# Kernel optimization log

Measured on AMD Instinct MI355X. Metric: run time of the kernel, lower is better.

The kernel has to match this reference:

```python
import jax, jax.numpy as jnp
import numpy as np

EPS = 1e-5

def conv1x1(x, w):
    # x: [B,C,H,W], w: [O,C] -> [B,O,H,W]
    return jnp.einsum('oc,bchw->bohw', w, x)

def bn(x, g, b, m, v):
    # inference batchnorm over channel dim 1
    scale = g / jnp.sqrt(v + EPS)
    return x * scale[None, :, None, None] + (b - m * scale)[None, :, None, None]

def setup_inputs() -> dict:
    key = jax.random.key(0)
    ks = jax.random.split(key, 20)
    B, Cin, S = 32, 256, 32
    C = Cin // 2
    rn = lambda k, sh: jax.random.normal(k, sh, dtype=jnp.float32)
    ru = lambda k, sh: jax.random.uniform(k, sh, dtype=jnp.float32)
    return {
        'x': rn(ks[0], (B, Cin, S, S)),
        'w1': rn(ks[1], (C, Cin)) * 0.05,
        'bn1_g': ru(ks[2], (C,)) + 0.5,
        'bn1_b': rn(ks[3], (C,)) * 0.1,
        'bn1_m': rn(ks[4], (C,)) * 0.1,
        'bn1_v': ru(ks[5], (C,)) + 0.5,
        'wq': rn(ks[6], (C, C)) * 0.05,
        'bq': rn(ks[7], (C,)) * 0.05,
        'wk': rn(ks[8], (C, C)) * 0.05,
        'bk': rn(ks[9], (C,)) * 0.05,
        'wv': rn(ks[10], (C, C)) * 0.05,
        'bv': rn(ks[11], (C,)) * 0.05,
        'rel_h': rn(ks[12], (1, C, S, 1)),
        'rel_w': rn(ks[13], (1, C, 1, S)),
        'w2': rn(ks[14], (Cin, C)) * 0.05,
        'bn2_g': ru(ks[15], (Cin,)) + 0.5,
        'bn2_b': rn(ks[16], (Cin,)) * 0.1,
        'bn2_m': rn(ks[17], (Cin,)) * 0.1,
        'bn2_v': ru(ks[18], (Cin,)) + 0.5,
    }

def reference(x, w1, bn1_g, bn1_b, bn1_m, bn1_v, wq, bq, wk, bk, wv, bv,
              rel_h, rel_w, w2, bn2_g, bn2_b, bn2_m, bn2_v):
    # cv1: 1x1 conv -> BN -> SiLU
    x1 = jax.nn.silu(bn(conv1x1(x, w1), bn1_g, bn1_b, bn1_m, bn1_v))
    B, C, H, W = x1.shape
    N = H * W
    # q/k/v: 1x1 conv with bias, flattened to [B,C,N]
    q = (conv1x1(x1, wq) + bq[None, :, None, None]).reshape(B, C, N)
    k = (conv1x1(x1, wk) + bk[None, :, None, None]).reshape(B, C, N)
    v = (conv1x1(x1, wv) + bv[None, :, None, None]).reshape(B, C, N)
    # content-content: q^T k -> [B,N,N]
    content_content = jnp.einsum('bci,bcj->bij', q, k)
    # content-position: pos^T q -> [B,N,N]
    pos = (rel_h + rel_w).reshape(C, N)  # [C,N]
    content_position = jnp.einsum('ci,bcj->bij', pos, q)
    attention = jax.nn.softmax(content_content + content_position, axis=-1)
    # out[b,c,i] = sum_j v[b,c,j] * attention[b,i,j]
    out = jnp.einsum('bcj,bij->bci', v, attention).reshape(B, C, H, W)
    # cv2: 1x1 conv -> BN -> SiLU, plus residual shortcut
    y = jax.nn.silu(bn(conv1x1(out, w2), bn2_g, bn2_b, bn2_m, bn2_v))
    return x + y
```

## Files before the change

kernel.cpp:

```cpp
#include <hip/hip_runtime.h>
#include <stdint.h>

typedef __bf16 bf16x8 __attribute__((ext_vector_type(8)));
typedef float  f32x4  __attribute__((ext_vector_type(4)));
typedef float  f32x16 __attribute__((ext_vector_type(16)));

#define MFMA(a,b,c)   __builtin_amdgcn_mfma_f32_16x16x32_bf16((a),(b),(c),0,0,0)
#define MFMA32(a,b,c) __builtin_amdgcn_mfma_f32_32x32x16_bf16((a),(b),(c),0,0,0)

__device__ __forceinline__ short f2b(float x) {
  uint32_t u = __float_as_uint(x);
  uint32_t r = (u + 0x7fffu + ((u >> 16) & 1u)) >> 16;
  return (short)r;
}

__device__ __forceinline__ uint32_t cvtpk(float lo, float hi) {
  uint32_t w;
  asm("v_cvt_pk_bf16_f32 %0, %1, %2" : "=v"(w) : "v"(lo), "v"(hi));
  return w;
}

__device__ __forceinline__ void glds16(const void* g, void* l) {
  __builtin_amdgcn_global_load_lds(
      (const __attribute__((address_space(1))) void*)(uintptr_t)g,
      (__attribute__((address_space(3))) void*)(uintptr_t)l, 16, 0, 0);
}

__global__ void k_prep(const float* __restrict__ w1, const float* __restrict__ wq,
                       const float* __restrict__ wk, const float* __restrict__ wv,
                       const float* __restrict__ w2,
                       const float* __restrict__ relh, const float* __restrict__ relw,
                       const float* __restrict__ g1, const float* __restrict__ b1,
                       const float* __restrict__ m1, const float* __restrict__ v1,
                       const float* __restrict__ g2, const float* __restrict__ b2,
                       const float* __restrict__ m2, const float* __restrict__ v2,
                       short* __restrict__ w1b, short* __restrict__ wqb,
                       short* __restrict__ wkb, short* __restrict__ wvb,
                       short* __restrict__ w2b, short* __restrict__ posT,
                       float* __restrict__ bnc) {
  int i = blockIdx.x * 256 + threadIdx.x;
  if (i < 32768) { w1b[i] = f2b(w1[i]); return; }
  i -= 32768;
  if (i < 16384) { wqb[i] = f2b(wq[i]); return; }
  i -= 16384;
  if (i < 16384) { wkb[i] = f2b(wk[i]); return; }
  i -= 16384;
  if (i < 16384) { wvb[i] = f2b(wv[i]); return; }
  i -= 16384;
  if (i < 32768) { w2b[i] = f2b(w2[i]); return; }
  i -= 32768;
  if (i < 131072) {
    int n = i >> 7, c = i & 127;
    int h = n >> 5, w = n & 31;
    posT[i] = f2b(relh[c * 32 + h] + relw[c * 32 + w]);
    return;
  }
  i -= 131072;
  if (i < 128) { float s = g1[i] * rsqrtf(v1[i] + 1e-5f); bnc[i] = s; bnc[128 + i] = b1[i] - m1[i] * s; return; }
  i -= 128;
  if (i < 256) { float s = g2[i] * rsqrtf(v2[i] + 1e-5f); bnc[256 + i] = s; bnc[512 + i] = b2[i] - m2[i] * s; return; }
}

__launch_bounds__(256)
__global__ void k_cq(const float* __restrict__ x, const short* __restrict__ w1b,
                     const short* __restrict__ wqb, const short* __restrict__ wkb,
                     const short* __restrict__ wvb, const float* __restrict__ bnc,
                     const float* __restrict__ bq, const float* __restrict__ bk,
                     const float* __restrict__ bv,
                     short* __restrict__ qT, short* __restrict__ kT,
                     short* __restrict__ vv) {
  __shared__ __align__(16) short Al[128 * 40];
  __shared__ __align__(16) short Bl[64 * 40];
  __shared__ __align__(16) short X1[64 * 136];
  const int bx = blockIdx.x;
  const int b = bx >> 4;
  const int n0 = (bx & 15) << 6;
  const int tid = threadIdx.x;
  const int wid = tid >> 6, lane = tid & 63;
  const int wr = wid >> 1, wc = wid & 1;
  const int cpr = lane & 15, g = lane >> 4;
  const float* xb = x + (size_t)b * (256 * 1024);

  {
    f32x4 acc[4][2] = {};
    for (int kk = 0; kk < 8; ++kk) {
#pragma unroll
      for (int it = 0; it < 2; ++it) {
        int f = tid + it * 256;
        int row = f >> 2, c8 = f & 3;
        *reinterpret_cast<uint4*>(&Al[row * 40 + c8 * 8]) =
            *reinterpret_cast<const uint4*>(&w1b[row * 256 + kk * 32 + c8 * 8]);
      }
#pragma unroll
      for (int it = 0; it < 2; ++it) {
        int f = tid + it * 256;
        int ci = f >> 4, c4 = f & 15;
        float4 v4 = *reinterpret_cast<const float4*>(&xb[(size_t)(kk * 32 + ci) * 1024 + n0 + c4 * 4]);
        int nb = c4 * 4;
        Bl[(nb + 0) * 40 + ci] = f2b(v4.x);
        Bl[(nb + 1) * 40 + ci] = f2b(v4.y);
        Bl[(nb + 2) * 40 + ci] = f2b(v4.z);
        Bl[(nb + 3) * 40 + ci] = f2b(v4.w);
      }
      __syncthreads();
      bf16x8 af[4], bfr[2];
#pragma unroll
      for (int mf = 0; mf < 4; ++mf)
        af[mf] = *reinterpret_cast<const bf16x8*>(&Al[(wr * 64 + mf * 16 + cpr) * 40 + g * 8]);
#pragma unroll
      for (int nf = 0; nf < 2; ++nf)
        bfr[nf] = *reinterpret_cast<const bf16x8*>(&Bl[(wc * 32 + nf * 16 + cpr) * 40 + g * 8]);
#pragma unroll
      for (int mf = 0; mf < 4; ++mf)
#pragma unroll
        for (int nf = 0; nf < 2; ++nf)
          acc[mf][nf] = MFMA(af[mf], bfr[nf], acc[mf][nf]);
      __syncthreads();
    }
#pragma unroll
    for (int mf = 0; mf < 4; ++mf) {
      int m0 = wr * 64 + mf * 16 + g * 4;
#pragma unroll
      for (int nf = 0; nf < 2; ++nf) {
        int nl = wc * 32 + nf * 16 + cpr;
        union { short s[4]; uint2 u; } pk;
#pragma unroll
        for (int r = 0; r < 4; ++r) {
          int c = m0 + r;
          float z = acc[mf][nf][r] * bnc[c] + bnc[128 + c];
          pk.s[r] = f2b(z / (1.f + __expf(-z)));
        }
        *reinterpret_cast<uint2*>(&X1[nl * 136 + m0]) = pk.u;
      }
    }
  }
  __syncthreads();

  for (int which = 0; which < 3; ++which) {
    const short* W = which == 0 ? wqb : which == 1 ? wkb : wvb;
    const float* bias = which == 0 ? bq : which == 1 ? bk : bv;
    f32x4 acc[4][2] = {};
    for (int kk = 0; kk < 4; ++kk) {
#pragma unroll
      for (int it = 0; it < 2; ++it) {
        int f = tid + it * 256;
        int row = f >> 2, c8 = f & 3;
        *reinterpret_cast<uint4*>(&Al[row * 40 + c8 * 8]) =
            *reinterpret_cast<const uint4*>(&W[row * 128 + kk * 32 + c8 * 8]);
      }
      __syncthreads();
      bf16x8 af[4], bfr[2];
#pragma unroll
      for (int mf = 0; mf < 4; ++mf)
        af[mf] = *reinterpret_cast<const bf16x8*>(&Al[(wr * 64 + mf * 16 + cpr) * 40 + g * 8]);
#pragma unroll
      for (int nf = 0; nf < 2; ++nf)
        bfr[nf] = *reinterpret_cast<const bf16x8*>(&X1[(wc * 32 + nf * 16 + cpr) * 136 + kk * 32 + g * 8]);
#pragma unroll
      for (int mf = 0; mf < 4; ++mf)
#pragma unroll
        for (int nf = 0; nf < 2; ++nf)
          acc[mf][nf] = MFMA(af[mf], bfr[nf], acc[mf][nf]);
      __syncthreads();
    }
#pragma unroll
    for (int mf = 0; mf < 4; ++mf) {
      int m0 = wr * 64 + mf * 16 + g * 4;
#pragma unroll
      for (int nf = 0; nf < 2; ++nf) {
        int n = n0 + wc * 32 + nf * 16 + cpr;
        if (which < 2) {
          union { short s4[4]; uint2 u; } pk;
#pragma unroll
          for (int r = 0; r < 4; ++r)
            pk.s4[r] = f2b(acc[mf][nf][r] + bias[m0 + r]);
          short* dst = which == 0 ? qT : kT;
          *reinterpret_cast<uint2*>(&dst[((size_t)b * 1024 + n) * 128 + m0]) = pk.u;
        } else {
#pragma unroll
          for (int r = 0; r < 4; ++r) {
            int c = m0 + r;
            vv[((size_t)b * 128 + c) * 1024 + n] = f2b(acc[mf][nf][r] + bias[c]);
          }
        }
      }
    }
  }
}

__launch_bounds__(512, 1)
__global__ void k_attn(const short* __restrict__ qT, const short* __restrict__ kT,
                       const short* __restrict__ vv, const short* __restrict__ posT,
                       const short* __restrict__ w2b, const float* __restrict__ bnc,
                       const float* __restrict__ x, float* __restrict__ out) {
  __shared__ __align__(16) char smem[100864];
  short* KhB0 = (short*)smem;
  short* KhB1 = (short*)(smem + 32768);
  short* VtB0 = (short*)(smem + 65536);
  short* VtB1 = (short*)(smem + 65536 + 16384);
  float*    Obuf  = (float*)smem;
  uint16_t* ObufB = (uint16_t*)(smem + 66048);
  float*    mlf   = (float*)(smem + 98816);

  const int bx0 = blockIdx.x;
  const int lbx = ((bx0 & 7) << 5) | (bx0 >> 3);
  const int b  = lbx >> 3;
  const int i0 = (lbx & 7) << 7;
  const int tid = threadIdx.x;
  const int wid = tid >> 6, lane = tid & 63;
  const int rl = lane & 31, hi = lane >> 5;
  const int jh = wid >> 2, iq = wid & 3;
  const size_t bN = (size_t)b * 1024;

  const short* srcK[4];
  const short* srcV[2];
#pragma unroll
  for (int it = 0; it < 4; ++it) {
    int gq = it * 512 + tid;
    int row = gq >> 5, p = gq & 31;
    int l = p ^ (row & 7);
    srcK[it] = (l < 16) ? &kT[(bN + row) * 128 + l * 8]
                        : &qT[(bN + row) * 128 + (l - 16) * 8];
  }
#pragma unroll
  for (int it = 0; it < 2; ++it) {
    int gq = it * 512 + tid;
    int c = gq >> 3, p = gq & 7;
    int l = p ^ (c & 7);
    srcV[it] = &vv[((size_t)b * 128 + c) * 1024 + l * 8];
  }
#pragma unroll
  for (int it = 0; it < 4; ++it) glds16(srcK[it], &KhB0[(it * 512 + wid * 64) * 8]);
#pragma unroll
  for (int it = 0; it < 2; ++it) glds16(srcV[it], &VtB0[(it * 512 + wid * 64) * 8]);

  bf16x8 qf[16];
  {
    const int irow = i0 + iq * 32 + rl;
#pragma unroll
    for (int ks = 0; ks < 8; ++ks)
      qf[ks] = *reinterpret_cast<const bf16x8*>(&qT[(bN + irow) * 128 + ks * 16 + hi * 8]);
#pragma unroll
    for (int ks = 8; ks < 16; ++ks)
      qf[ks] = *reinterpret_cast<const bf16x8*>(&posT[(size_t)irow * 128 + (ks - 8) * 16 + hi * 8]);
  }
  __syncthreads();

  f32x16 oacc[4] = {};
  float mrow = -3e38f, lrow = 0.f;

  for (int jt = 0; jt < 16; ++jt) {
    const int cur = jt & 1;
    if (jt < 15) {
      short* KhN = cur ? KhB0 : KhB1;
      short* VtN = cur ? VtB0 : VtB1;
#pragma unroll
      for (int it = 0; it < 4; ++it)
        glds16(srcK[it] + ((jt + 1) << 13), &KhN[(it * 512 + wid * 64) * 8]);
#pragma unroll
      for (int it = 0; it < 2; ++it)
        glds16(srcV[it] + ((jt + 1) << 6), &VtN[(it * 512 + wid * 64) * 8]);
    }
    const short* KhC = cur ? KhB1 : KhB0;
    const short* VtC = cur ? VtB1 : VtB0;

    f32x16 s0 = {}, s1 = {};
    {
      const int rb = (jh * 32 + rl) * 256;
      __builtin_amdgcn_s_setprio(1);
#pragma unroll
      for (int ks = 0; ks < 16; ++ks) {
        int p = ((ks << 1) | hi) ^ (rl & 7);
        bf16x8 kf = *reinterpret_cast<const bf16x8*>(&KhC[rb + p * 8]);
        if (ks & 1) s1 = MFMA32(kf, qf[ks], s1);
        else        s0 = MFMA32(kf, qf[ks], s0);
      }
      __builtin_amdgcn_s_setprio(0);
    }
    float t[16];
#pragma unroll
    for (int r = 0; r < 16; ++r) t[r] = s0[r] + s1[r];
    float mx = t[0];
#pragma unroll
    for (int r = 1; r < 16; ++r) mx = fmaxf(mx, t[r]);
    mx = fmaxf(mx, __shfl_xor(mx, 32));
    float pr[16];
    float ps = 0.f;
    if (__all(mx <= mrow + 8.f)) {
#pragma unroll
      for (int r = 0; r < 16; ++r) { pr[r] = __expf(t[r] - mrow); ps += pr[r]; }
      ps += __shfl_xor(ps, 32);
      lrow += ps;
    } else {
      float mnew = fmaxf(mrow, mx);
      float sc = __expf(mrow - mnew);
#pragma unroll
      for (int r = 0; r < 16; ++r) { pr[r] = __expf(t[r] - mnew); ps += pr[r]; }
      ps += __shfl_xor(ps, 32);
      lrow = lrow * sc + ps;
      mrow = mnew;
#pragma unroll
      for (int ct = 0; ct < 4; ++ct)
#pragma unroll
        for (int r = 0; r < 16; ++r) oacc[ct][r] *= sc;
    }
    uint32_t own[8], rcv[8];
#pragma unroll
    for (int idx = 0; idx < 8; ++idx) own[idx] = cvtpk(pr[2 * idx], pr[2 * idx + 1]);
#pragma unroll
    for (int idx = 0; idx < 8; ++idx) rcv[idx] = __shfl_xor((int)own[idx], 32);
#pragma unroll
    for (int js = 0; js < 2; ++js) {
      union { uint32_t u[4]; bf16x8 v; } pa;
      pa.u[0] = hi ? rcv[4 * js + 2] : own[4 * js + 0];
      pa.u[1] = hi ? rcv[4 * js + 3] : own[4 * js + 1];
      pa.u[2] = hi ? own[4 * js + 2] : rcv[4 * js + 0];
      pa.u[3] = hi ? own[4 * js + 3] : rcv[4 * js + 1];
      __builtin_amdgcn_s_setprio(1);
#pragma unroll
      for (int ct = 0; ct < 4; ++ct) {
        int c = ct * 32 + rl;
        int p = ((jh << 2) | (js << 1) | hi) ^ (rl & 7);
        bf16x8 vf = *reinterpret_cast<const bf16x8*>(&VtC[c * 64 + p * 8]);
        oacc[ct] = MFMA32(vf, pa.v, oacc[ct]);
      }
      __builtin_amdgcn_s_setprio(0);
    }
    __syncthreads();
  }

  if (lane < 32) {
    mlf[wid * 64 + rl]      = mrow;
    mlf[wid * 64 + 32 + rl] = lrow;
  }
  __syncthreads();
  float scl;
  {
    const int pid = wid ^ 4;
    float mp = mlf[pid * 64 + rl];
    float lp = mlf[pid * 64 + 32 + rl];
    float M  = fmaxf(mrow, mp);
    float f  = __expf(mrow - M);
    float fp = __expf(mp - M);
    scl = f / (lrow * f + lp * fp);
  }
  bf16x8 af2[8];
#pragma unroll
  for (int ks = 0; ks < 8; ++ks)
    af2[ks] = *reinterpret_cast<const bf16x8*>(&w2b[(size_t)(wid * 32 + rl) * 128 + ks * 16 + hi * 8]);
  __syncthreads();

  const int row = iq * 32 + rl;
  if (jh == 0) {
#pragma unroll
    for (int ct = 0; ct < 4; ++ct)
#pragma unroll
      for (int r = 0; r < 16; ++r) {
        int c = ct * 32 + (r & 3) + 8 * (r >> 2) + 4 * hi;
        Obuf[row * 129 + c] = oacc[ct][r] * scl;
      }
  }
  __syncthreads();
  if (jh == 1) {
    uint32_t* OW = (uint32_t*)ObufB;
#pragma unroll
    for (int ct = 0; ct < 4; ++ct) {
      float mg[16];
#pragma unroll
      for (int r = 0; r < 16; ++r) {
        int c = ct * 32 + (r & 3) + 8 * (r >> 2) + 4 * hi;
        mg[r] = Obuf[row * 129 + c] + oacc[ct][r] * scl;
      }
#pragma unroll
      for (int m = 0; m < 8; ++m) {
        int c0 = ct * 32 + ((2 * m) & 3) + 8 * ((2 * m) >> 2) + 4 * hi;
        int gI = c0 >> 3, wo = (c0 & 7) >> 1;
        int gS = gI ^ (row & 15);
        OW[row * 64 + gS * 4 + wo] = cvtpk(mg[2 * m], mg[2 * m + 1]);
      }
    }
  }
  __syncthreads();

  f32x16 a2[4] = {};
#pragma unroll
  for (int it = 0; it < 4; ++it) {
    const int r2 = it * 32 + rl;
    __builtin_amdgcn_s_setprio(1);
#pragma unroll
    for (int ks = 0; ks < 8; ++ks) {
      int gS = ((ks << 1) | hi) ^ (r2 & 15);
      bf16x8 bf = *reinterpret_cast<const bf16x8*>(&ObufB[r2 * 128 + gS * 8]);
      a2[it] = MFMA32(af2[ks], bf, a2[it]);
    }
    __builtin_amdgcn_s_setprio(0);
  }
  float bsc[16], bsh[16];
#pragma unroll
  for (int r = 0; r < 16; ++r) {
    int co = wid * 32 + (r & 3) + 8 * (r >> 2) + 4 * hi;
    bsc[r] = bnc[256 + co];
    bsh[r] = bnc[512 + co];
  }
#pragma unroll
  for (int it = 0; it < 4; ++it) {
#pragma unroll
    for (int r = 0; r < 16; ++r) {
      int co = wid * 32 + (r & 3) + 8 * (r >> 2) + 4 * hi;
      size_t idx = ((size_t)b * 256 + co) * 1024 + i0 + it * 32 + rl;
      float y = a2[it][r] * bsc[r] + bsh[r];
      out[idx] = x[idx] + y / (1.f + __expf(-y));
    }
  }
}

extern "C" void kernel_launch(void* const* d_in, const int* in_sizes, int n_in,
                              void* d_out, int out_size, void* d_ws, size_t ws_size,
                              hipStream_t stream) {
  (void)in_sizes; (void)n_in; (void)out_size; (void)ws_size;
  const float* x    = (const float*)d_in[0];
  const float* w1   = (const float*)d_in[1];
  const float* g1   = (const float*)d_in[2];
  const float* b1   = (const float*)d_in[3];
  const float* m1   = (const float*)d_in[4];
  const float* v1   = (const float*)d_in[5];
  const float* wq   = (const float*)d_in[6];
  const float* bq   = (const float*)d_in[7];
  const float* wk   = (const float*)d_in[8];
  const float* bk   = (const float*)d_in[9];
  const float* wv   = (const float*)d_in[10];
  const float* bv   = (const float*)d_in[11];
  const float* relh = (const float*)d_in[12];
  const float* relw = (const float*)d_in[13];
  const float* w2   = (const float*)d_in[14];
  const float* g2   = (const float*)d_in[15];
  const float* b2   = (const float*)d_in[16];
  const float* m2   = (const float*)d_in[17];
  const float* v2   = (const float*)d_in[18];
  float* out = (float*)d_out;

  char* ws = (char*)d_ws;
  const size_t OFF_W1B  = 0;
  const size_t OFF_WQB  = 65536;
  const size_t OFF_WKB  = 98304;
  const size_t OFF_WVB  = 131072;
  const size_t OFF_W2B  = 163840;
  const size_t OFF_POST = 229376;
  const size_t OFF_BN   = 491520;
  const size_t OFF_QT   = 494592;
  const size_t OFF_KT   = OFF_QT + 8388608;
  const size_t OFF_V    = OFF_KT + 8388608;

  short* w1b  = (short*)(ws + OFF_W1B);
  short* wqb  = (short*)(ws + OFF_WQB);
  short* wkb  = (short*)(ws + OFF_WKB);
  short* wvb  = (short*)(ws + OFF_WVB);
  short* w2b  = (short*)(ws + OFF_W2B);
  short* posT = (short*)(ws + OFF_POST);
  float* bnc  = (float*)(ws + OFF_BN);
  short* qT   = (short*)(ws + OFF_QT);
  short* kT   = (short*)(ws + OFF_KT);
  short* vv   = (short*)(ws + OFF_V);

  k_prep<<<962, 256, 0, stream>>>(w1, wq, wk, wv, w2, relh, relw,
                                  g1, b1, m1, v1, g2, b2, m2, v2,
                                  w1b, wqb, wkb, wvb, w2b, posT, bnc);
  k_cq<<<512, 256, 0, stream>>>(x, w1b, wqb, wkb, wvb, bnc, bq, bk, bv, qT, kT, vv);
  k_attn<<<256, 512, 0, stream>>>(qT, kT, vv, posT, w2b, bnc, x, out);
}
```

Measured before the change: 90.97 us.

## Factor position term into separable row and column bias tables

Because pos = rel_h + rel_w, the content-position term splits into U[h_i, j] + W[w_i, j], with U = rel_h^T q and W = rel_w^T q. A new kernel computes these small 32xN tables per batch. The attention kernel then adds them as biases instead of running a second 128-deep contraction. This halves the K-dimension of the score MFMA and the K tile traffic per step. In exchange it adds a kernel launch and per-step fp32 loads of U and W from global memory.

```diff
diff --git a/kernel.cpp b/kernel.cpp
--- a/kernel.cpp
+++ b/kernel.cpp
@@ -36,8 +36,8 @@
                        const float* __restrict__ m2, const float* __restrict__ v2,
                        short* __restrict__ w1b, short* __restrict__ wqb,
                        short* __restrict__ wkb, short* __restrict__ wvb,
-                       short* __restrict__ w2b, short* __restrict__ posT,
-                       float* __restrict__ bnc) {
+                       short* __restrict__ w2b, short* __restrict__ rhT,
+                       short* __restrict__ rwT, float* __restrict__ bnc) {
   int i = blockIdx.x * 256 + threadIdx.x;
   if (i < 32768) { w1b[i] = f2b(w1[i]); return; }
   i -= 32768;
@@ -49,13 +49,10 @@
   i -= 16384;
   if (i < 32768) { w2b[i] = f2b(w2[i]); return; }
   i -= 32768;
-  if (i < 131072) {
-    int n = i >> 7, c = i & 127;
-    int h = n >> 5, w = n & 31;
-    posT[i] = f2b(relh[c * 32 + h] + relw[c * 32 + w]);
-    return;
-  }
-  i -= 131072;
+  if (i < 4096) { int h = i >> 7, c = i & 127; rhT[i] = f2b(relh[c * 32 + h]); return; }
+  i -= 4096;
+  if (i < 4096) { int w = i >> 7, c = i & 127; rwT[i] = f2b(relw[c * 32 + w]); return; }
+  i -= 4096;
   if (i < 128) { float s = g1[i] * rsqrtf(v1[i] + 1e-5f); bnc[i] = s; bnc[128 + i] = b1[i] - m1[i] * s; return; }
   i -= 128;
   if (i < 256) { float s = g2[i] * rsqrtf(v2[i] + 1e-5f); bnc[256 + i] = s; bnc[512 + i] = b2[i] - m2[i] * s; return; }
@@ -188,16 +185,61 @@
   }
 }
 
+__launch_bounds__(256)
+__global__ void k_uw(const short* __restrict__ qT, const short* __restrict__ rhT,
+                     const short* __restrict__ rwT, float* __restrict__ Ug,
+                     float* __restrict__ Wg) {
+  __shared__ float Tb[4][32][36];
+  const int bx = blockIdx.x;
+  const int b = bx >> 3;
+  const int jblk = (bx & 7) << 7;
+  const int tid = threadIdx.x;
+  const int wid = tid >> 6, lane = tid & 63;
+  const int rl = lane & 31, hi = lane >> 5;
+  const int j0 = jblk + wid * 32;
+  const size_t bN = (size_t)b * 1024;
+
+  bf16x8 qfrag[8];
+#pragma unroll
+  for (int ks = 0; ks < 8; ++ks)
+    qfrag[ks] = *reinterpret_cast<const bf16x8*>(&qT[(bN + j0 + rl) * 128 + ks * 16 + hi * 8]);
+
+#pragma unroll
+  for (int m = 0; m < 2; ++m) {
+    const short* R = m ? rwT : rhT;
+    float* Og = m ? Wg : Ug;
+    f32x16 d = {};
+#pragma unroll
+    for (int ks = 0; ks < 8; ++ks) {
+      bf16x8 a = *reinterpret_cast<const bf16x8*>(&R[(size_t)rl * 128 + ks * 16 + hi * 8]);
+      d = MFMA32(a, qfrag[ks], d);
+    }
+#pragma unroll
+    for (int r = 0; r < 16; ++r)
+      Tb[wid][(r & 3) + 8 * (r >> 2) + 4 * hi][rl] = d[r];
+    __syncthreads();
+#pragma unroll
+    for (int it = 0; it < 4; ++it) {
+      int gq = it * 64 + lane;
+      int h = gq >> 3, j4 = gq & 7;
+      float4 v = *reinterpret_cast<const float4*>(&Tb[wid][h][j4 * 4]);
+      *reinterpret_cast<float4*>(&Og[((size_t)b * 32 + h) * 1024 + j0 + j4 * 4]) = v;
+    }
+    __syncthreads();
+  }
+}
+
 __launch_bounds__(512, 1)
 __global__ void k_attn(const short* __restrict__ qT, const short* __restrict__ kT,
-                       const short* __restrict__ vv, const short* __restrict__ posT,
+                       const short* __restrict__ vv, const float* __restrict__ Ug,
+                       const float* __restrict__ Wg,
                        const short* __restrict__ w2b, const float* __restrict__ bnc,
                        const float* __restrict__ x, float* __restrict__ out) {
   __shared__ __align__(16) char smem[100864];
   short* KhB0 = (short*)smem;
-  short* KhB1 = (short*)(smem + 32768);
-  short* VtB0 = (short*)(smem + 65536);
-  short* VtB1 = (short*)(smem + 65536 + 16384);
+  short* KhB1 = (short*)(smem + 16384);
+  short* VtB0 = (short*)(smem + 32768);
+  short* VtB1 = (short*)(smem + 49152);
   float*    Obuf  = (float*)smem;
   uint16_t* ObufB = (uint16_t*)(smem + 66048);
   float*    mlf   = (float*)(smem + 98816);
@@ -211,16 +253,16 @@
   const int rl = lane & 31, hi = lane >> 5;
   const int jh = wid >> 2, iq = wid & 3;
   const size_t bN = (size_t)b * 1024;
-
-  const short* srcK[4];
+  const int hI = ((lbx & 7) << 2) + iq;
+
+  const short* srcK[2];
   const short* srcV[2];
 #pragma unroll
-  for (int it = 0; it < 4; ++it) {
+  for (int it = 0; it < 2; ++it) {
     int gq = it * 512 + tid;
-    int row = gq >> 5, p = gq & 31;
+    int row = gq >> 4, p = gq & 15;
     int l = p ^ (row & 7);
-    srcK[it] = (l < 16) ? &kT[(bN + row) * 128 + l * 8]
-                        : &qT[(bN + row) * 128 + (l - 16) * 8];
+    srcK[it] = &kT[(bN + row) * 128 + l * 8];
   }
 #pragma unroll
   for (int it = 0; it < 2; ++it) {
@@ -230,32 +272,37 @@
     srcV[it] = &vv[((size_t)b * 128 + c) * 1024 + l * 8];
   }
 #pragma unroll
-  for (int it = 0; it < 4; ++it) glds16(srcK[it], &KhB0[(it * 512 + wid * 64) * 8]);
+  for (int it = 0; it < 2; ++it) glds16(srcK[it], &KhB0[(it * 512 + wid * 64) * 8]);
 #pragma unroll
   for (int it = 0; it < 2; ++it) glds16(srcV[it], &VtB0[(it * 512 + wid * 64) * 8]);
 
-  bf16x8 qf[16];
+  bf16x8 qf[8];
   {
     const int irow = i0 + iq * 32 + rl;
 #pragma unroll
     for (int ks = 0; ks < 8; ++ks)
       qf[ks] = *reinterpret_cast<const bf16x8*>(&qT[(bN + irow) * 128 + ks * 16 + hi * 8]);
-#pragma unroll
-    for (int ks = 8; ks < 16; ++ks)
-      qf[ks] = *reinterpret_cast<const bf16x8*>(&posT[(size_t)irow * 128 + (ks - 8) * 16 + hi * 8]);
   }
   __syncthreads();
 
   f32x16 oacc[4] = {};
   float mrow = -3e38f, lrow = 0.f;
+  const float* Urow = &Ug[((size_t)b * 32 + hI) * 1024 + (jh << 5) + (hi << 2)];
+  const float* Wrow = &Wg[((size_t)b * 32 + rl) * 1024 + (jh << 5) + (hi << 2)];
 
   for (int jt = 0; jt < 16; ++jt) {
     const int cur = jt & 1;
+    f32x4 u4[4], w4[4];
+#pragma unroll
+    for (int g2 = 0; g2 < 4; ++g2) {
+      u4[g2] = *reinterpret_cast<const f32x4*>(&Urow[(jt << 6) + g2 * 8]);
+      w4[g2] = *reinterpret_cast<const f32x4*>(&Wrow[(jt << 6) + g2 * 8]);
+    }
     if (jt < 15) {
       short* KhN = cur ? KhB0 : KhB1;
       short* VtN = cur ? VtB0 : VtB1;
 #pragma unroll
-      for (int it = 0; it < 4; ++it)
+      for (int it = 0; it < 2; ++it)
         glds16(srcK[it] + ((jt + 1) << 13), &KhN[(it * 512 + wid * 64) * 8]);
 #pragma unroll
       for (int it = 0; it < 2; ++it)
@@ -266,10 +313,10 @@
 
     f32x16 s0 = {}, s1 = {};
     {
-      const int rb = (jh * 32 + rl) * 256;
+      const int rb = (jh * 32 + rl) * 128;
       __builtin_amdgcn_s_setprio(1);
 #pragma unroll
-      for (int ks = 0; ks < 16; ++ks) {
+      for (int ks = 0; ks < 8; ++ks) {
         int p = ((ks << 1) | hi) ^ (rl & 7);
         bf16x8 kf = *reinterpret_cast<const bf16x8*>(&KhC[rb + p * 8]);
         if (ks & 1) s1 = MFMA32(kf, qf[ks], s1);
@@ -279,7 +326,8 @@
     }
     float t[16];
 #pragma unroll
-    for (int r = 0; r < 16; ++r) t[r] = s0[r] + s1[r];
+    for (int r = 0; r < 16; ++r)
+      t[r] = s0[r] + s1[r] + u4[r >> 2][r & 3] + w4[r >> 2][r & 3];
     float mx = t[0];
 #pragma unroll
     for (int r = 1; r < 16; ++r) mx = fmaxf(mx, t[r]);
@@ -445,26 +493,33 @@
   const size_t OFF_WKB  = 98304;
   const size_t OFF_WVB  = 131072;
   const size_t OFF_W2B  = 163840;
-  const size_t OFF_POST = 229376;
+  const size_t OFF_RHT  = 229376;
+  const size_t OFF_RWT  = 237568;
   const size_t OFF_BN   = 491520;
   const size_t OFF_QT   = 494592;
   const size_t OFF_KT   = OFF_QT + 8388608;
   const size_t OFF_V    = OFF_KT + 8388608;
+  const size_t OFF_UG   = OFF_V + 8388608;
+  const size_t OFF_WG   = OFF_UG + 4194304;
 
   short* w1b  = (short*)(ws + OFF_W1B);
   short* wqb  = (short*)(ws + OFF_WQB);
   short* wkb  = (short*)(ws + OFF_WKB);
   short* wvb  = (short*)(ws + OFF_WVB);
   short* w2b  = (short*)(ws + OFF_W2B);
-  short* posT = (short*)(ws + OFF_POST);
+  short* rhT  = (short*)(ws + OFF_RHT);
+  short* rwT  = (short*)(ws + OFF_RWT);
   float* bnc  = (float*)(ws + OFF_BN);
   short* qT   = (short*)(ws + OFF_QT);
   short* kT   = (short*)(ws + OFF_KT);
   short* vv   = (short*)(ws + OFF_V);
-
-  k_prep<<<962, 256, 0, stream>>>(w1, wq, wk, wv, w2, relh, relw,
+  float* Ug   = (float*)(ws + OFF_UG);
+  float* Wg   = (float*)(ws + OFF_WG);
+
+  k_prep<<<482, 256, 0, stream>>>(w1, wq, wk, wv, w2, relh, relw,
                                   g1, b1, m1, v1, g2, b2, m2, v2,
-                                  w1b, wqb, wkb, wvb, w2b, posT, bnc);
+                                  w1b, wqb, wkb, wvb, w2b, rhT, rwT, bnc);
   k_cq<<<512, 256, 0, stream>>>(x, w1b, wqb, wkb, wvb, bnc, bq, bk, bv, qT, kT, vv);
-  k_attn<<<256, 512, 0, stream>>>(qT, kT, vv, posT, w2b, bnc, x, out);
-}
+  k_uw<<<256, 256, 0, stream>>>(qT, rhT, rwT, Ug, Wg);
+  k_attn<<<256, 512, 0, stream>>>(qT, kT, vv, Ug, Wg, w2b, bnc, x, out);
+}
```

New measurement: 93.68 us. +3.0%, slower.
